# Kernel optimization log

Hardware: AMD Instinct MI355X
Metric: run time of the kernel (lower is better)

The kernel has to match this reference:

```python
import jax, jax.numpy as jnp
import numpy as np

VOCAB, EMB, H, OUT = 32000, 512, 1024, 32000
SEQ, B = 512, 64

def setup_inputs() -> dict:
    key = jax.random.key(0)
    ks = jax.random.split(key, 16)
    sc = lambda *s: 1.0 / np.sqrt(s[-1])
    return {
        "x": jax.random.randint(ks[0], (B,), 0, VOCAB),
        "encoder_states": jax.random.normal(ks[1], (SEQ, B, 2 * H), jnp.float32),
        "hidden": jax.random.normal(ks[2], (1, B, H), jnp.float32),
        "cell": jax.random.normal(ks[3], (1, B, H), jnp.float32),
        "emb_table": jax.random.normal(ks[4], (VOCAB, EMB), jnp.float32),
        "energy_W": jax.random.normal(ks[5], (1, 3 * H), jnp.float32) * sc(1, 3 * H),
        "energy_b": jnp.zeros((1,), jnp.float32),
        "W_ih": jax.random.normal(ks[6], (4 * H, 2 * H + EMB), jnp.float32) * sc(1, H),
        "W_hh": jax.random.normal(ks[7], (4 * H, H), jnp.float32) * sc(1, H),
        "b_ih": jnp.zeros((4 * H,), jnp.float32),
        "b_hh": jnp.zeros((4 * H,), jnp.float32),
        "fc_W": jax.random.normal(ks[8], (OUT, H), jnp.float32) * sc(1, H),
        "fc_b": jnp.zeros((OUT,), jnp.float32),
    }

def reference(x, encoder_states, hidden, cell, emb_table, energy_W, energy_b,
              W_ih, W_hh, b_ih, b_hh, fc_W, fc_b):
    S = encoder_states.shape[0]
    emb = emb_table[x]                                     # [B, E] (dropout is identity at p=0)
    h_rep = jnp.broadcast_to(hidden, (S,) + hidden.shape[1:])   # [S, B, H]
    cat = jnp.concatenate([h_rep, encoder_states], axis=2)      # [S, B, 3H]
    energy = jax.nn.relu(jnp.einsum('sbk,ok->sbo', cat, energy_W) + energy_b)  # [S, B, 1]
    attn = jax.nn.softmax(energy[..., 0], axis=0)                # softmax over seq dim -> [S, B]
    context = jnp.einsum('sb,sbd->bd', attn, encoder_states)     # [B, 2H]
    rnn_in = jnp.concatenate([context, emb], axis=1)             # [B, 2H+E]
    gates = rnn_in @ W_ih.T + b_ih + hidden[0] @ W_hh.T + b_hh   # [B, 4H]
    i, f, g, o = jnp.split(gates, 4, axis=1)
    i, f, o = jax.nn.sigmoid(i), jax.nn.sigmoid(f), jax.nn.sigmoid(o)
    g = jnp.tanh(g)
    c_new = f * cell[0] + i * g
    h_new = o * jnp.tanh(c_new)
    preds = h_new @ fc_W.T + fc_b                                # [B, OUT]
    return preds, h_new[None], c_new[None]
```

## Files before the change

kernel.cpp:

```cpp
#include <hip/hip_runtime.h>

#define S_LEN 512
#define BATCH 64
#define HDIM  1024
#define TWOH  2048
#define EMB   512
#define KDIM  2560
#define KTOT  3584
#define VOUT  32000

#define WS_MS    64
#define WS_CTX   2112
#define WS_GP    WS_CTX
#define WS_RNNB  (WS_CTX + 64*16*2048)
#define WS_HB16  (WS_RNNB + 114688)

typedef __attribute__((ext_vector_type(8))) short bf16x8;
typedef __attribute__((ext_vector_type(4))) float f32x4;

__device__ __forceinline__ float sigmoidf_(float x) { return 1.f/(1.f+__expf(-x)); }

__device__ __forceinline__ unsigned short f2bf(float f) {
  union { float f; unsigned u; } v; v.f = f;
  return (unsigned short)((v.u + 0x7fffu + ((v.u >> 16) & 1u)) >> 16);
}

__device__ __forceinline__ bf16x8 cvt_frag(const float4& a, const float4& b) {
  bf16x8 r;
  r[0] = (short)f2bf(a.x); r[1] = (short)f2bf(a.y);
  r[2] = (short)f2bf(a.z); r[3] = (short)f2bf(a.w);
  r[4] = (short)f2bf(b.x); r[5] = (short)f2bf(b.y);
  r[6] = (short)f2bf(b.z); r[7] = (short)f2bf(b.w);
  return r;
}

__global__ __launch_bounds__(256) void k_attn(const float* __restrict__ enc,
                                              const float* __restrict__ eW,
                                              const float* __restrict__ eb,
                                              const float* __restrict__ hidden,
                                              float* __restrict__ ws_ms,
                                              float* __restrict__ ws_ctx) {
  __shared__ float lds_ms[4][2];
  __shared__ float lds_ctx[4][2048];
  const int lane  = threadIdx.x & 63;
  const int wave  = threadIdx.x >> 6;
  const int chunk = blockIdx.x;
  const int b     = blockIdx.y;

  float hba = 0.f;
  for (int k = lane; k < HDIM; k += 64) hba += hidden[b*HDIM + k] * eW[k];
#pragma unroll
  for (int st = 32; st >= 1; st >>= 1) hba += __shfl_xor(hba, st, 64);
  const float hb = hba + eb[0];

  float4 w4[8];
#pragma unroll
  for (int k = 0; k < 8; ++k)
    w4[k] = *reinterpret_cast<const float4*>(eW + HDIM + 4*lane + 256*k);

  const int s0 = chunk*32 + wave*8;
  const float* base = enc + ((size_t)(s0*BATCH + b))*TWOH + 4*lane;

  float m = 0.f, ssum = 0.f;
  float4 ctx[8];
#pragma unroll
  for (int k = 0; k < 8; ++k) ctx[k] = make_float4(0.f, 0.f, 0.f, 0.f);

  float4 va[8], vb[8];
#pragma unroll
  for (int k = 0; k < 8; ++k) va[k] = *reinterpret_cast<const float4*>(base + 256*k);

#define ATTN_STEP(VCUR, VNXT, I)                                              \
  {                                                                           \
    if ((I) < 7) {                                                            \
      const float* pn = base + (size_t)((I)+1)*BATCH*TWOH;                    \
      _Pragma("unroll")                                                       \
      for (int k = 0; k < 8; ++k)                                             \
        VNXT[k] = *reinterpret_cast<const float4*>(pn + 256*k);               \
    }                                                                         \
    float a = 0.f;                                                            \
    _Pragma("unroll")                                                         \
    for (int k = 0; k < 8; ++k)                                               \
      a += VCUR[k].x*w4[k].x + VCUR[k].y*w4[k].y +                            \
           VCUR[k].z*w4[k].z + VCUR[k].w*w4[k].w;                             \
    _Pragma("unroll")                                                         \
    for (int st = 1; st < 64; st <<= 1) a += __shfl_xor(a, st, 64);           \
    const float e = fmaxf(a + hb, 0.f);                                       \
    if (e > m) {                                                              \
      const float sc = __expf(m - e);                                         \
      ssum = ssum*sc + 1.f;                                                   \
      _Pragma("unroll")                                                       \
      for (int k = 0; k < 8; ++k) {                                           \
        ctx[k].x = fmaf(ctx[k].x, sc, VCUR[k].x);                             \
        ctx[k].y = fmaf(ctx[k].y, sc, VCUR[k].y);                             \
        ctx[k].z = fmaf(ctx[k].z, sc, VCUR[k].z);                             \
        ctx[k].w = fmaf(ctx[k].w, sc, VCUR[k].w);                             \
      }                                                                       \
      m = e;                                                                  \
    } else {                                                                  \
      const float pw = __expf(e - m);                                         \
      ssum += pw;                                                             \
      _Pragma("unroll")                                                       \
      for (int k = 0; k < 8; ++k) {                                           \
        ctx[k].x = fmaf(pw, VCUR[k].x, ctx[k].x);                             \
        ctx[k].y = fmaf(pw, VCUR[k].y, ctx[k].y);                             \
        ctx[k].z = fmaf(pw, VCUR[k].z, ctx[k].z);                             \
        ctx[k].w = fmaf(pw, VCUR[k].w, ctx[k].w);                             \
      }                                                                       \
    }                                                                         \
  }

  ATTN_STEP(va, vb, 0)
  ATTN_STEP(vb, va, 1)
  ATTN_STEP(va, vb, 2)
  ATTN_STEP(vb, va, 3)
  ATTN_STEP(va, vb, 4)
  ATTN_STEP(vb, va, 5)
  ATTN_STEP(va, vb, 6)
  ATTN_STEP(vb, va, 7)
#undef ATTN_STEP

  if (lane == 0) { lds_ms[wave][0] = m; lds_ms[wave][1] = ssum; }
  __syncthreads();
  const float M = fmaxf(fmaxf(lds_ms[0][0], lds_ms[1][0]),
                        fmaxf(lds_ms[2][0], lds_ms[3][0]));
  const float wsc = __expf(m - M);
  float ssum_c = 0.f;
#pragma unroll
  for (int w = 0; w < 4; ++w) ssum_c += __expf(lds_ms[w][0] - M) * lds_ms[w][1];
#pragma unroll
  for (int k = 0; k < 8; ++k) {
    float4 c = ctx[k];
    c.x *= wsc; c.y *= wsc; c.z *= wsc; c.w *= wsc;
    *reinterpret_cast<float4*>(&lds_ctx[wave][4*lane + 256*k]) = c;
  }
  __syncthreads();
  float* outp = ws_ctx + ((size_t)b*16 + chunk)*TWOH;
  for (int d = threadIdx.x; d < TWOH; d += 256)
    outp[d] = lds_ctx[0][d] + lds_ctx[1][d] + lds_ctx[2][d] + lds_ctx[3][d];
  if (threadIdx.x == 0) {
    ws_ms[((size_t)b*16 + chunk)*2]     = M;
    ws_ms[((size_t)b*16 + chunk)*2 + 1] = ssum_c;
  }
}

__global__ __launch_bounds__(256) void k_combine(const float* __restrict__ ws_ms,
                                                 const float* __restrict__ ws_ctx,
                                                 const float* __restrict__ hidden,
                                                 const float* __restrict__ emb_table,
                                                 const int* __restrict__ x,
                                                 unsigned short* __restrict__ rnnB) {
  const int b = blockIdx.y;
  const int k = blockIdx.x*256 + threadIdx.x;
  unsigned short* rb = rnnB + (size_t)b*KTOT;

  if (k < TWOH) {
    float mc[16], sc[16];
#pragma unroll
    for (int c = 0; c < 16; ++c) {
      mc[c] = ws_ms[(b*16 + c)*2];
      sc[c] = ws_ms[(b*16 + c)*2 + 1];
    }
    float M = mc[0];
#pragma unroll
    for (int c = 1; c < 16; ++c) M = fmaxf(M, mc[c]);
    float wc[16], Ssum = 0.f;
#pragma unroll
    for (int c = 0; c < 16; ++c) { wc[c] = __expf(mc[c] - M); Ssum += wc[c]*sc[c]; }
    const float inv = 1.f / Ssum;
    float a = 0.f;
#pragma unroll
    for (int c = 0; c < 16; ++c) a += wc[c] * ws_ctx[((size_t)b*16 + c)*TWOH + k];
    rb[k] = f2bf(a * inv);
  } else if (k < KDIM) {
    const int xb = x[b];
    rb[k] = f2bf(emb_table[(size_t)xb*EMB + (k - TWOH)]);
  } else {
    rb[k] = f2bf(hidden[b*HDIM + (k - KDIM)]);
  }
}

__global__ __launch_bounds__(256) void k_gates(const unsigned short* __restrict__ rnnB,
                                               const float* __restrict__ W_ih,
                                               const float* __restrict__ W_hh,
                                               float* __restrict__ ws_gp) {
  const int lane = threadIdx.x & 63;
  const int wave = threadIdx.x >> 6;
  const int part = blockIdx.x & 7;
  const int rg   = blockIdx.x >> 3;
  const int row0 = rg*64 + wave*16;
  const int mlo  = lane & 15;
  const int kg   = lane >> 4;
  const int j    = row0 + mlo;
  const unsigned short* rp0 = rnnB + (size_t)mlo*KTOT;

  f32x4 acc0 = {0.f,0.f,0.f,0.f}, acc1 = acc0, acc2 = acc0, acc3 = acc0;

  float4  Aa[4], Ab[4];
  bf16x8  Ba[8], Bb[8];

#define G_LOAD(AW, BB, S)                                                     \
  {                                                                           \
    const int kb0 = part*448 + (S)*64;                                        \
    const int kb1 = kb0 + 32;                                                 \
    const float* ws0 = (kb0 < KDIM) ? (W_ih + (size_t)j*KDIM + kb0 + kg*8)    \
                                    : (W_hh + (size_t)j*HDIM + (kb0-KDIM) + kg*8); \
    const float* ws1 = (kb1 < KDIM) ? (W_ih + (size_t)j*KDIM + kb1 + kg*8)    \
                                    : (W_hh + (size_t)j*HDIM + (kb1-KDIM) + kg*8); \
    AW[0] = *reinterpret_cast<const float4*>(ws0);                            \
    AW[1] = *reinterpret_cast<const float4*>(ws0 + 4);                        \
    AW[2] = *reinterpret_cast<const float4*>(ws1);                            \
    AW[3] = *reinterpret_cast<const float4*>(ws1 + 4);                        \
    const size_t ko0 = (size_t)kb0 + kg*8;                                    \
    const size_t ko1 = (size_t)kb1 + kg*8;                                    \
    BB[0] = *reinterpret_cast<const bf16x8*>(rp0 + ko0);                      \
    BB[1] = *reinterpret_cast<const bf16x8*>(rp0 + 16*KTOT + ko0);            \
    BB[2] = *reinterpret_cast<const bf16x8*>(rp0 + 32*KTOT + ko0);            \
    BB[3] = *reinterpret_cast<const bf16x8*>(rp0 + 48*KTOT + ko0);            \
    BB[4] = *reinterpret_cast<const bf16x8*>(rp0 + ko1);                      \
    BB[5] = *reinterpret_cast<const bf16x8*>(rp0 + 16*KTOT + ko1);            \
    BB[6] = *reinterpret_cast<const bf16x8*>(rp0 + 32*KTOT + ko1);            \
    BB[7] = *reinterpret_cast<const bf16x8*>(rp0 + 48*KTOT + ko1);            \
  }

#define G_COMP(AW, BB)                                                        \
  {                                                                           \
    const bf16x8 af0 = cvt_frag(AW[0], AW[1]);                                \
    const bf16x8 af1 = cvt_frag(AW[2], AW[3]);                                \
    acc0 = __builtin_amdgcn_mfma_f32_16x16x32_bf16(af0, BB[0], acc0, 0, 0, 0);\
    acc1 = __builtin_amdgcn_mfma_f32_16x16x32_bf16(af0, BB[1], acc1, 0, 0, 0);\
    acc2 = __builtin_amdgcn_mfma_f32_16x16x32_bf16(af0, BB[2], acc2, 0, 0, 0);\
    acc3 = __builtin_amdgcn_mfma_f32_16x16x32_bf16(af0, BB[3], acc3, 0, 0, 0);\
    acc0 = __builtin_amdgcn_mfma_f32_16x16x32_bf16(af1, BB[4], acc0, 0, 0, 0);\
    acc1 = __builtin_amdgcn_mfma_f32_16x16x32_bf16(af1, BB[5], acc1, 0, 0, 0);\
    acc2 = __builtin_amdgcn_mfma_f32_16x16x32_bf16(af1, BB[6], acc2, 0, 0, 0);\
    acc3 = __builtin_amdgcn_mfma_f32_16x16x32_bf16(af1, BB[7], acc3, 0, 0, 0);\
  }

  G_LOAD(Aa, Ba, 0)
  G_LOAD(Ab, Bb, 1) G_COMP(Aa, Ba)
  G_LOAD(Aa, Ba, 2) G_COMP(Ab, Bb)
  G_LOAD(Ab, Bb, 3) G_COMP(Aa, Ba)
  G_LOAD(Aa, Ba, 4) G_COMP(Ab, Bb)
  G_LOAD(Ab, Bb, 5) G_COMP(Aa, Ba)
  G_LOAD(Aa, Ba, 6) G_COMP(Ab, Bb)
  G_COMP(Aa, Ba)
#undef G_LOAD
#undef G_COMP

  const int mbase = row0 + kg*4;
#define G_ST(ACC, N)                                                          \
  {                                                                           \
    _Pragma("unroll")                                                         \
    for (int jj = 0; jj < 4; ++jj)                                            \
      ws_gp[((size_t)part*4096 + mbase + jj)*64 + ((N)*16 + mlo)] = ACC[jj];  \
  }
  G_ST(acc0, 0) G_ST(acc1, 1) G_ST(acc2, 2) G_ST(acc3, 3)
#undef G_ST
}

__global__ __launch_bounds__(256) void k_lstm(const float* __restrict__ ws_gp,
                                              const float* __restrict__ b_ih,
                                              const float* __restrict__ b_hh,
                                              const float* __restrict__ cell,
                                              float* __restrict__ out_h,
                                              float* __restrict__ out_c,
                                              unsigned short* __restrict__ hB) {
  const int id = blockIdx.x*256 + threadIdx.x;
  const int h = id >> 6, b = id & 63;
  float g[4];
#pragma unroll
  for (int gg = 0; gg < 4; ++gg) {
    const int j = gg*1024 + h;
    float v = b_ih[j] + b_hh[j];
#pragma unroll
    for (int p = 0; p < 8; ++p) v += ws_gp[((size_t)p*4096 + j)*64 + b];
    g[gg] = v;
  }
  const float iv = sigmoidf_(g[0]);
  const float fv = sigmoidf_(g[1]);
  const float gv = tanhf(g[2]);
  const float ov = sigmoidf_(g[3]);
  const float cold = cell[b*HDIM + h];
  const float cn = fmaf(fv, cold, iv*gv);
  const float hn = ov * tanhf(cn);
  out_h[b*HDIM + h] = hn;
  out_c[b*HDIM + h] = cn;
  hB[(size_t)b*HDIM + h] = f2bf(hn);
}

__global__ __launch_bounds__(256) void k_fc(const unsigned short* __restrict__ hB,
                                            const float* __restrict__ fc_W,
                                            const float* __restrict__ fc_b,
                                            float* __restrict__ preds) {
  const int lane = threadIdx.x & 63;
  const int wave = threadIdx.x >> 6;
  const int row0 = (blockIdx.x*4 + wave)*16;
  const int mlo  = lane & 15;
  const int kg   = lane >> 4;

  const float* wrow = fc_W + (size_t)(row0 + mlo)*HDIM + kg*8;
  const unsigned short* hp = hB + (size_t)mlo*HDIM + kg*8;

  f32x4 acc0 = {0.f,0.f,0.f,0.f}, acc1 = acc0, acc2 = acc0, acc3 = acc0;

  float4  Aa[4], Ab[4];
  bf16x8  Ba[8], Bb[8];

#define FC_LOAD(AW, BB, K0)                                                   \
  {                                                                           \
    AW[0] = *reinterpret_cast<const float4*>(wrow + (K0));                    \
    AW[1] = *reinterpret_cast<const float4*>(wrow + (K0) + 4);                \
    AW[2] = *reinterpret_cast<const float4*>(wrow + (K0) + 32);               \
    AW[3] = *reinterpret_cast<const float4*>(wrow + (K0) + 36);               \
    BB[0] = *reinterpret_cast<const bf16x8*>(hp + (K0));                      \
    BB[1] = *reinterpret_cast<const bf16x8*>(hp + 16*HDIM + (K0));            \
    BB[2] = *reinterpret_cast<const bf16x8*>(hp + 32*HDIM + (K0));            \
    BB[3] = *reinterpret_cast<const bf16x8*>(hp + 48*HDIM + (K0));            \
    BB[4] = *reinterpret_cast<const bf16x8*>(hp + (K0) + 32);                 \
    BB[5] = *reinterpret_cast<const bf16x8*>(hp + 16*HDIM + (K0) + 32);       \
    BB[6] = *reinterpret_cast<const bf16x8*>(hp + 32*HDIM + (K0) + 32);       \
    BB[7] = *reinterpret_cast<const bf16x8*>(hp + 48*HDIM + (K0) + 32);       \
  }

#define FC_COMP(AW, BB)                                                       \
  {                                                                           \
    const bf16x8 af0 = cvt_frag(AW[0], AW[1]);                                \
    const bf16x8 af1 = cvt_frag(AW[2], AW[3]);                                \
    acc0 = __builtin_amdgcn_mfma_f32_16x16x32_bf16(af0, BB[0], acc0, 0, 0, 0);\
    acc1 = __builtin_amdgcn_mfma_f32_16x16x32_bf16(af0, BB[1], acc1, 0, 0, 0);\
    acc2 = __builtin_amdgcn_mfma_f32_16x16x32_bf16(af0, BB[2], acc2, 0, 0, 0);\
    acc3 = __builtin_amdgcn_mfma_f32_16x16x32_bf16(af0, BB[3], acc3, 0, 0, 0);\
    acc0 = __builtin_amdgcn_mfma_f32_16x16x32_bf16(af1, BB[4], acc0, 0, 0, 0);\
    acc1 = __builtin_amdgcn_mfma_f32_16x16x32_bf16(af1, BB[5], acc1, 0, 0, 0);\
    acc2 = __builtin_amdgcn_mfma_f32_16x16x32_bf16(af1, BB[6], acc2, 0, 0, 0);\
    acc3 = __builtin_amdgcn_mfma_f32_16x16x32_bf16(af1, BB[7], acc3, 0, 0, 0);\
  }

  FC_LOAD(Aa, Ba, 0)
  FC_LOAD(Ab, Bb, 64)  FC_COMP(Aa, Ba)
  FC_LOAD(Aa, Ba, 128) FC_COMP(Ab, Bb)
  FC_LOAD(Ab, Bb, 192) FC_COMP(Aa, Ba)
  FC_LOAD(Aa, Ba, 256) FC_COMP(Ab, Bb)
  FC_LOAD(Ab, Bb, 320) FC_COMP(Aa, Ba)
  FC_LOAD(Aa, Ba, 384) FC_COMP(Ab, Bb)
  FC_LOAD(Ab, Bb, 448) FC_COMP(Aa, Ba)
  FC_LOAD(Aa, Ba, 512) FC_COMP(Ab, Bb)
  FC_LOAD(Ab, Bb, 576) FC_COMP(Aa, Ba)
  FC_LOAD(Aa, Ba, 640) FC_COMP(Ab, Bb)
  FC_LOAD(Ab, Bb, 704) FC_COMP(Aa, Ba)
  FC_LOAD(Aa, Ba, 768) FC_COMP(Ab, Bb)
  FC_LOAD(Ab, Bb, 832) FC_COMP(Aa, Ba)
  FC_LOAD(Aa, Ba, 896) FC_COMP(Ab, Bb)
  FC_LOAD(Ab, Bb, 960) FC_COMP(Aa, Ba)
  FC_COMP(Ab, Bb)
#undef FC_LOAD
#undef FC_COMP

  const int mbase = row0 + kg*4;
  const float4 bias = make_float4(fc_b[mbase], fc_b[mbase+1],
                                  fc_b[mbase+2], fc_b[mbase+3]);
#define FC_STORE(ACC, N)                                                      \
  {                                                                           \
    float4 st = make_float4(ACC[0] + bias.x, ACC[1] + bias.y,                 \
                            ACC[2] + bias.z, ACC[3] + bias.w);                \
    *reinterpret_cast<float4*>(preds + (size_t)((N)*16 + mlo)*VOUT + mbase) = st; \
  }
  FC_STORE(acc0, 0) FC_STORE(acc1, 1) FC_STORE(acc2, 2) FC_STORE(acc3, 3)
#undef FC_STORE
}

extern "C" void kernel_launch(void* const* d_in, const int* in_sizes, int n_in,
                              void* d_out, int out_size, void* d_ws, size_t ws_size,
                              hipStream_t stream) {
  const int*   x      = (const int*)  d_in[0];
  const float* enc    = (const float*)d_in[1];
  const float* hidden = (const float*)d_in[2];
  const float* cell   = (const float*)d_in[3];
  const float* embt   = (const float*)d_in[4];
  const float* eW     = (const float*)d_in[5];
  const float* eb     = (const float*)d_in[6];
  const float* W_ih   = (const float*)d_in[7];
  const float* W_hh   = (const float*)d_in[8];
  const float* b_ih   = (const float*)d_in[9];
  const float* b_hh   = (const float*)d_in[10];
  const float* fc_W   = (const float*)d_in[11];
  const float* fc_b   = (const float*)d_in[12];

  float* out   = (float*)d_out;
  float* preds = out;
  float* out_h = out + (size_t)BATCH*VOUT;
  float* out_c = out_h + BATCH*HDIM;
  float* ws    = (float*)d_ws;
  unsigned short* rnnB = (unsigned short*)(ws + WS_RNNB);
  unsigned short* hB   = (unsigned short*)(ws + WS_HB16);

  k_attn<<<dim3(16, 64), 256, 0, stream>>>(enc, eW, eb, hidden, ws + WS_MS, ws + WS_CTX);
  k_combine<<<dim3(14, 64), 256, 0, stream>>>(ws + WS_MS, ws + WS_CTX, hidden, embt, x, rnnB);
  k_gates<<<512, 256, 0, stream>>>(rnnB, W_ih, W_hh, ws + WS_GP);
  k_lstm<<<256, 256, 0, stream>>>(ws + WS_GP, b_ih, b_hh, cell, out_h, out_c, hB);
  k_fc<<<500, 256, 0, stream>>>(hB, fc_W, fc_b, preds);
}
```

Measured before the change: 145.9 us.

## Stage fc_W tiles through swizzled double-buffered LDS with coalesced loads

The FC kernel now loads fc_W chunks cooperatively with coalesced float4 loads, converts them to bf16, and writes them into a double-buffered, XOR-swizzled LDS tile. Each wave then reads its MFMA A fragments from LDS, replacing the strided per-lane global loads from the previous register double-buffering. This aims to improve global access coalescing on the 131MB weight stream. In exchange it adds a __syncthreads per k-chunk and LDS traffic, which could limit latency hiding in a bandwidth-bound kernel.

```diff
diff --git a/kernel.cpp b/kernel.cpp
--- a/kernel.cpp
+++ b/kernel.cpp
@@ -293,78 +293,90 @@
                                             const float* __restrict__ fc_W,
                                             const float* __restrict__ fc_b,
                                             float* __restrict__ preds) {
-  const int lane = threadIdx.x & 63;
-  const int wave = threadIdx.x >> 6;
-  const int row0 = (blockIdx.x*4 + wave)*16;
+  __shared__ unsigned short lds_a[2][64*64];
+  const int tid  = threadIdx.x;
+  const int lane = tid & 63;
+  const int wave = tid >> 6;
+  const int row0b = blockIdx.x * 64;
   const int mlo  = lane & 15;
   const int kg   = lane >> 4;
-
-  const float* wrow = fc_W + (size_t)(row0 + mlo)*HDIM + kg*8;
+  const int srow = tid >> 4;
+  const int scol = (tid & 15) * 4;
+
   const unsigned short* hp = hB + (size_t)mlo*HDIM + kg*8;
 
   f32x4 acc0 = {0.f,0.f,0.f,0.f}, acc1 = acc0, acc2 = acc0, acc3 = acc0;
-
-  float4  Aa[4], Ab[4];
-  bf16x8  Ba[8], Bb[8];
-
-#define FC_LOAD(AW, BB, K0)                                                   \
-  {                                                                           \
-    AW[0] = *reinterpret_cast<const float4*>(wrow + (K0));                    \
-    AW[1] = *reinterpret_cast<const float4*>(wrow + (K0) + 4);                \
-    AW[2] = *reinterpret_cast<const float4*>(wrow + (K0) + 32);               \
-    AW[3] = *reinterpret_cast<const float4*>(wrow + (K0) + 36);               \
-    BB[0] = *reinterpret_cast<const bf16x8*>(hp + (K0));                      \
-    BB[1] = *reinterpret_cast<const bf16x8*>(hp + 16*HDIM + (K0));            \
-    BB[2] = *reinterpret_cast<const bf16x8*>(hp + 32*HDIM + (K0));            \
-    BB[3] = *reinterpret_cast<const bf16x8*>(hp + 48*HDIM + (K0));            \
-    BB[4] = *reinterpret_cast<const bf16x8*>(hp + (K0) + 32);                 \
-    BB[5] = *reinterpret_cast<const bf16x8*>(hp + 16*HDIM + (K0) + 32);       \
-    BB[6] = *reinterpret_cast<const bf16x8*>(hp + 32*HDIM + (K0) + 32);       \
-    BB[7] = *reinterpret_cast<const bf16x8*>(hp + 48*HDIM + (K0) + 32);       \
-  }
-
-#define FC_COMP(AW, BB)                                                       \
-  {                                                                           \
-    const bf16x8 af0 = cvt_frag(AW[0], AW[1]);                                \
-    const bf16x8 af1 = cvt_frag(AW[2], AW[3]);                                \
-    acc0 = __builtin_amdgcn_mfma_f32_16x16x32_bf16(af0, BB[0], acc0, 0, 0, 0);\
-    acc1 = __builtin_amdgcn_mfma_f32_16x16x32_bf16(af0, BB[1], acc1, 0, 0, 0);\
-    acc2 = __builtin_amdgcn_mfma_f32_16x16x32_bf16(af0, BB[2], acc2, 0, 0, 0);\
-    acc3 = __builtin_amdgcn_mfma_f32_16x16x32_bf16(af0, BB[3], acc3, 0, 0, 0);\
-    acc0 = __builtin_amdgcn_mfma_f32_16x16x32_bf16(af1, BB[4], acc0, 0, 0, 0);\
-    acc1 = __builtin_amdgcn_mfma_f32_16x16x32_bf16(af1, BB[5], acc1, 0, 0, 0);\
-    acc2 = __builtin_amdgcn_mfma_f32_16x16x32_bf16(af1, BB[6], acc2, 0, 0, 0);\
-    acc3 = __builtin_amdgcn_mfma_f32_16x16x32_bf16(af1, BB[7], acc3, 0, 0, 0);\
-  }
-
-  FC_LOAD(Aa, Ba, 0)
-  FC_LOAD(Ab, Bb, 64)  FC_COMP(Aa, Ba)
-  FC_LOAD(Aa, Ba, 128) FC_COMP(Ab, Bb)
-  FC_LOAD(Ab, Bb, 192) FC_COMP(Aa, Ba)
-  FC_LOAD(Aa, Ba, 256) FC_COMP(Ab, Bb)
-  FC_LOAD(Ab, Bb, 320) FC_COMP(Aa, Ba)
-  FC_LOAD(Aa, Ba, 384) FC_COMP(Ab, Bb)
-  FC_LOAD(Ab, Bb, 448) FC_COMP(Aa, Ba)
-  FC_LOAD(Aa, Ba, 512) FC_COMP(Ab, Bb)
-  FC_LOAD(Ab, Bb, 576) FC_COMP(Aa, Ba)
-  FC_LOAD(Aa, Ba, 640) FC_COMP(Ab, Bb)
-  FC_LOAD(Ab, Bb, 704) FC_COMP(Aa, Ba)
-  FC_LOAD(Aa, Ba, 768) FC_COMP(Ab, Bb)
-  FC_LOAD(Ab, Bb, 832) FC_COMP(Aa, Ba)
-  FC_LOAD(Aa, Ba, 896) FC_COMP(Ab, Bb)
-  FC_LOAD(Ab, Bb, 960) FC_COMP(Aa, Ba)
-  FC_COMP(Ab, Bb)
-#undef FC_LOAD
-#undef FC_COMP
-
-  const int mbase = row0 + kg*4;
+  float4 st[4];
+
+#define FC_GLOAD(C)                                                           \
+  _Pragma("unroll")                                                           \
+  for (int jj = 0; jj < 4; ++jj)                                              \
+    st[jj] = *reinterpret_cast<const float4*>(                                \
+        fc_W + (size_t)(row0b + srow + jj*16)*HDIM + (C)*64 + scol);
+
+#define FC_SWRITE(BUF)                                                        \
+  _Pragma("unroll")                                                           \
+  for (int jj = 0; jj < 4; ++jj) {                                            \
+    const int r = srow + jj*16;                                               \
+    unsigned short tmp[4];                                                    \
+    tmp[0] = f2bf(st[jj].x); tmp[1] = f2bf(st[jj].y);                         \
+    tmp[2] = f2bf(st[jj].z); tmp[3] = f2bf(st[jj].w);                         \
+    const int boff = r*128 + ((scol*2) ^ ((r & 7) << 4));                     \
+    *reinterpret_cast<uint2*>(reinterpret_cast<char*>(lds_a[BUF]) + boff) =   \
+        *reinterpret_cast<const uint2*>(tmp);                                 \
+  }
+
+  FC_GLOAD(0)
+  FC_SWRITE(0)
+  __syncthreads();
+
+  int cur = 0;
+  const int arow = wave*16 + mlo;
+  const int abase = arow*128;
+  const int asw  = (arow & 7) << 4;
+
+  for (int c = 0; c < 16; ++c) {
+    if (c < 15) FC_GLOAD(c+1)
+
+    const bf16x8 af0 = *reinterpret_cast<const bf16x8*>(
+        reinterpret_cast<const char*>(lds_a[cur]) + abase + ((kg*16) ^ asw));
+    const bf16x8 af1 = *reinterpret_cast<const bf16x8*>(
+        reinterpret_cast<const char*>(lds_a[cur]) + abase + ((64 + kg*16) ^ asw));
+
+    const int K0 = c*64;
+    const bf16x8 b00 = *reinterpret_cast<const bf16x8*>(hp + K0);
+    const bf16x8 b10 = *reinterpret_cast<const bf16x8*>(hp + 16*HDIM + K0);
+    const bf16x8 b20 = *reinterpret_cast<const bf16x8*>(hp + 32*HDIM + K0);
+    const bf16x8 b30 = *reinterpret_cast<const bf16x8*>(hp + 48*HDIM + K0);
+    const bf16x8 b01 = *reinterpret_cast<const bf16x8*>(hp + K0 + 32);
+    const bf16x8 b11 = *reinterpret_cast<const bf16x8*>(hp + 16*HDIM + K0 + 32);
+    const bf16x8 b21 = *reinterpret_cast<const bf16x8*>(hp + 32*HDIM + K0 + 32);
+    const bf16x8 b31 = *reinterpret_cast<const bf16x8*>(hp + 48*HDIM + K0 + 32);
+
+    acc0 = __builtin_amdgcn_mfma_f32_16x16x32_bf16(af0, b00, acc0, 0, 0, 0);
+    acc1 = __builtin_amdgcn_mfma_f32_16x16x32_bf16(af0, b10, acc1, 0, 0, 0);
+    acc2 = __builtin_amdgcn_mfma_f32_16x16x32_bf16(af0, b20, acc2, 0, 0, 0);
+    acc3 = __builtin_amdgcn_mfma_f32_16x16x32_bf16(af0, b30, acc3, 0, 0, 0);
+    acc0 = __builtin_amdgcn_mfma_f32_16x16x32_bf16(af1, b01, acc0, 0, 0, 0);
+    acc1 = __builtin_amdgcn_mfma_f32_16x16x32_bf16(af1, b11, acc1, 0, 0, 0);
+    acc2 = __builtin_amdgcn_mfma_f32_16x16x32_bf16(af1, b21, acc2, 0, 0, 0);
+    acc3 = __builtin_amdgcn_mfma_f32_16x16x32_bf16(af1, b31, acc3, 0, 0, 0);
+
+    if (c < 15) FC_SWRITE(cur ^ 1)
+    __syncthreads();
+    cur ^= 1;
+  }
+#undef FC_GLOAD
+#undef FC_SWRITE
+
+  const int mbase = row0b + wave*16 + kg*4;
   const float4 bias = make_float4(fc_b[mbase], fc_b[mbase+1],
                                   fc_b[mbase+2], fc_b[mbase+3]);
 #define FC_STORE(ACC, N)                                                      \
   {                                                                           \
-    float4 st = make_float4(ACC[0] + bias.x, ACC[1] + bias.y,                 \
-                            ACC[2] + bias.z, ACC[3] + bias.w);                \
-    *reinterpret_cast<float4*>(preds + (size_t)((N)*16 + mlo)*VOUT + mbase) = st; \
+    float4 stv = make_float4(ACC[0] + bias.x, ACC[1] + bias.y,                \
+                             ACC[2] + bias.z, ACC[3] + bias.w);               \
+    *reinterpret_cast<float4*>(preds + (size_t)((N)*16 + mlo)*VOUT + mbase) = stv; \
   }
   FC_STORE(acc0, 0) FC_STORE(acc1, 1) FC_STORE(acc2, 2) FC_STORE(acc3, 3)
 #undef FC_STORE
```

Result: faster. 139.0 us (-4.7%).
